# Kernel optimization log

Hardware: AMD Instinct MI355X
Metric: run time of the kernel (lower is better)

## Reference

```python
import jax, jax.numpy as jnp
import numpy as np

B, T, C, H = 2, 2048, 1024, 16
D = C // H
EPS = 1e-5
ROPE_BASE = 10000.0


def _rope_tables(t, d, base=ROPE_BASE):
    half = d // 2
    inv_freq = 1.0 / (base ** (jnp.arange(half, dtype=jnp.float32) / half))
    freqs = jnp.arange(t, dtype=jnp.float32)[:, None] * inv_freq[None, :]  # [T, D/2]
    emb = jnp.concatenate([freqs, freqs], axis=-1)  # [T, D]
    return jnp.cos(emb), jnp.sin(emb)


def _rotate_half(x):
    a, b = jnp.split(x, 2, axis=-1)
    return jnp.concatenate([-b, a], axis=-1)


def setup_inputs() -> dict:
    key = jax.random.key(0)
    k0, k1, k2 = jax.random.split(key, 3)
    s = 0.02  # typical init scale
    return {
        "x": jax.random.normal(k0, (B, T, C), jnp.float32),
        "attention_mask": jnp.ones((B, T), jnp.int32),
        "w_qkv": jax.random.normal(k1, (3 * C, C), jnp.float32) * s,
        "b_qkv": jnp.zeros((3 * C,), jnp.float32),
        "w_o": jax.random.normal(k2, (C, C), jnp.float32) * s,
        "b_o": jnp.zeros((C,), jnp.float32),
        "rms_w": jnp.ones((C,), jnp.float32),
    }


def reference(x, attention_mask, w_qkv, b_qkv, w_o, b_o, rms_w):
    b, t, c = x.shape
    h = H
    d = c // h
    # RMSNorm
    xn = x * jax.lax.rsqrt(jnp.mean(x * x, axis=-1, keepdims=True) + EPS) * rms_w
    # fused QKV projection -> [B, T, 3, H, D]
    qkv = (jnp.einsum('btc,oc->bto', xn, w_qkv) + b_qkv).reshape(b, t, 3, h, d)
    q, k, v = qkv[:, :, 0], qkv[:, :, 1], qkv[:, :, 2]
    # RoPE (position_ids = arange(T))
    cos, sin = _rope_tables(t, d)
    cos = cos[None, :, None, :]  # [1, T, 1, D]
    sin = sin[None, :, None, :]
    q = q * cos + _rotate_half(q) * sin
    k = k * cos + _rotate_half(k) * sin
    # causal attention (flash_attn_func semantics: scale 1/sqrt(d), causal)
    scores = jnp.einsum('bqhd,bkhd->bhqk', q, k) / jnp.sqrt(jnp.float32(d))
    causal = jnp.tril(jnp.ones((t, t), dtype=bool))
    scores = jnp.where(causal[None, None], scores, jnp.float32(-1e30))
    attn = jax.nn.softmax(scores, axis=-1)
    out = jnp.einsum('bhqk,bkhd->bqhd', attn, v).reshape(b, t, c)
    return jnp.einsum('btc,oc->bto', out, w_o) + b_o
```

## Files before the change

### kernel.cpp

```cpp
#include <hip/hip_runtime.h>
#include <math.h>

constexpr int Bb = 2;
constexpr int Tt = 2048;
constexpr int Cc = 1024;
constexpr int Hh = 16;
constexpr int M_ROWS = Bb * Tt;
constexpr float EPSV = 1e-5f;

typedef __attribute__((ext_vector_type(4))) float f32x4;
typedef __attribute__((ext_vector_type(8))) __bf16 bf16x8;
using u16 = unsigned short;

union Frag8 {
    u16 u[8];
    unsigned int ui[4];
    uint4 v;
    bf16x8 b;
};

__device__ __forceinline__ u16 f2bf(float f) {
    union { float f; unsigned int u; } c;
    c.f = f;
    unsigned int r = (c.u + 0x7fffu + ((c.u >> 16) & 1u)) >> 16;
    return (u16)r;
}
__device__ __forceinline__ float bf2f(u16 u) {
    union { unsigned int i; float f; } c;
    c.i = ((unsigned int)u) << 16;
    return c.f;
}

__device__ __forceinline__ void gload_lds16(const void* g, void* l) {
    __builtin_amdgcn_global_load_lds(
        (__attribute__((address_space(1))) void*)const_cast<void*>(g),
        (__attribute__((address_space(3))) void*)l, 16, 0, 0);
}

__global__ __launch_bounds__(64) void rope_tables_k(float* __restrict__ cosT,
                                                    float* __restrict__ sinT) {
    int tid = threadIdx.x;
    int t = blockIdx.x * 2 + (tid >> 5);
    int j = tid & 31;
    float inv = exp2f(-(float)j * (log2f(10000.0f) / 32.0f));
    float a = (float)t * inv;
    cosT[t * 32 + j] = cosf(a);
    sinT[t * 32 + j] = sinf(a);
}

__global__ __launch_bounds__(256) void f2bf_arr_k(const float* __restrict__ in,
                                                  u16* __restrict__ out) {
    int i = (blockIdx.x * 256 + threadIdx.x) * 4;
    float4 v = *(const float4*)&in[i];
    ushort4 o;
    o.x = f2bf(v.x); o.y = f2bf(v.y); o.z = f2bf(v.z); o.w = f2bf(v.w);
    *(ushort4*)&out[i] = o;
}

__global__ __launch_bounds__(256) void rmsnorm_k(const float* __restrict__ x,
                                                 const float* __restrict__ w,
                                                 u16* __restrict__ xn) {
    int row = blockIdx.x;
    int tid = threadIdx.x;
    const float* xr = x + (size_t)row * Cc;
    float4 v = *(const float4*)&xr[tid * 4];
    float ss = v.x * v.x + v.y * v.y + v.z * v.z + v.w * v.w;
    #pragma unroll
    for (int off = 32; off > 0; off >>= 1) ss += __shfl_down(ss, off);
    __shared__ float ws_[4];
    if ((tid & 63) == 0) ws_[tid >> 6] = ss;
    __syncthreads();
    float tot = ws_[0] + ws_[1] + ws_[2] + ws_[3];
    float r = rsqrtf(tot * (1.0f / (float)Cc) + EPSV);
    float4 wv = *(const float4*)&w[tid * 4];
    ushort4 o;
    o.x = f2bf(v.x * r * wv.x);
    o.y = f2bf(v.y * r * wv.y);
    o.z = f2bf(v.z * r * wv.z);
    o.w = f2bf(v.w * r * wv.w);
    *(ushort4*)&xn[(size_t)row * Cc + tid * 4] = o;
}

template<bool BF16OUT>
__global__ __launch_bounds__(256) void gemm_mfma_k(const u16* __restrict__ A,
                                                   const u16* __restrict__ W,
                                                   const float* __restrict__ bias,
                                                   void* __restrict__ Ov,
                                                   int M, int N, int K) {
    __shared__ __align__(16) u16 As[128 * 64];
    __shared__ __align__(16) u16 Bs[128 * 64];

    const int tid = threadIdx.x;
    const int w = tid >> 6;
    const int l = tid & 63;
    const int wr = w >> 1;
    const int wc = w & 1;
    const int q = l & 15;
    const int g = l >> 4;

    const int m0 = blockIdx.y * 128;
    const int n0 = blockIdx.x * 128;

    const int srow_in = l >> 3;
    const int p_chunk = l & 7;

    f32x4 acc[4][4];
    #pragma unroll
    for (int i = 0; i < 4; ++i)
        #pragma unroll
        for (int j = 0; j < 4; ++j)
            acc[i][j] = (f32x4){0.f, 0.f, 0.f, 0.f};

    const int nkt = K >> 6;
    for (int kt = 0; kt < nkt; ++kt) {
        const int k0 = kt << 6;
        __syncthreads();
        #pragma unroll
        for (int s = 0; s < 4; ++s) {
            int blk = s * 4 + w;
            int r = blk * 8 + srow_in;
            int c = p_chunk ^ (r & 7);
            gload_lds16(A + (size_t)(m0 + r) * K + k0 + c * 8, &As[blk * 512]);
            gload_lds16(W + (size_t)(n0 + r) * K + k0 + c * 8, &Bs[blk * 512]);
        }
        __syncthreads();

        #pragma unroll
        for (int kk = 0; kk < 2; ++kk) {
            Frag8 af[4], bf[4];
            const int ca = kk * 4 + g;
            #pragma unroll
            for (int i = 0; i < 4; ++i) {
                int ra = wr * 64 + i * 16 + q;
                af[i] = *(const Frag8*)&As[ra * 64 + ((ca ^ (ra & 7)) * 8)];
                int rb = wc * 64 + i * 16 + q;
                bf[i] = *(const Frag8*)&Bs[rb * 64 + ((ca ^ (rb & 7)) * 8)];
            }
            #pragma unroll
            for (int i = 0; i < 4; ++i)
                #pragma unroll
                for (int j = 0; j < 4; ++j)
                    acc[i][j] = __builtin_amdgcn_mfma_f32_16x16x32_bf16(
                        af[i].b, bf[j].b, acc[i][j], 0, 0, 0);
        }
    }

    #pragma unroll
    for (int i = 0; i < 4; ++i) {
        int row = m0 + wr * 64 + i * 16 + g * 4;
        #pragma unroll
        for (int j = 0; j < 4; ++j) {
            int col = n0 + wc * 64 + j * 16 + q;
            float bb = bias[col];
            #pragma unroll
            for (int r2 = 0; r2 < 4; ++r2) {
                float val = acc[i][j][r2] + bb;
                if (BF16OUT)
                    ((u16*)Ov)[(size_t)(row + r2) * N + col] = f2bf(val);
                else
                    ((float*)Ov)[(size_t)(row + r2) * N + col] = val;
            }
        }
    }
}

__global__ __launch_bounds__(256) void rope_pack_k(const u16* __restrict__ qkv,
                                                   const float* __restrict__ cosT,
                                                   const float* __restrict__ sinT,
                                                   u16* __restrict__ Qb,
                                                   u16* __restrict__ Kb,
                                                   u16* __restrict__ Vt) {
    const int t0 = blockIdx.x * 64;
    const int h = blockIdx.y, b = blockIdx.z;
    const int t = threadIdx.x;
    const int bh = b * Hh + h;
    __shared__ u16 Vs[64 * 64];
    constexpr float QSC = 0.125f * 1.44269504089f;

    {
        int row = t >> 2, d16 = (t & 3) * 16;
        const u16* vp = qkv + (size_t)(b * Tt + t0 + row) * 3072 + 2048 + h * 64 + d16;
        *(uint4*)&Vs[row * 64 + d16]     = *(const uint4*)vp;
        *(uint4*)&Vs[row * 64 + d16 + 8] = *(const uint4*)(vp + 8);
    }

    {
        int row = t >> 2, d0 = (t & 3) * 8;
        size_t rb = (size_t)(b * Tt + t0 + row) * 3072 + h * 64;
        const u16* qp = qkv + rb;
        const u16* kp = qkv + rb + 1024;
        Frag8 qlo, qhi, klo, khi;
        qlo.v = *(const uint4*)&qp[d0];
        qhi.v = *(const uint4*)&qp[d0 + 32];
        klo.v = *(const uint4*)&kp[d0];
        khi.v = *(const uint4*)&kp[d0 + 32];
        const float* cp = &cosT[(t0 + row) * 32 + d0];
        const float* sp = &sinT[(t0 + row) * 32 + d0];
        float4 c0 = *(const float4*)cp, c1 = *(const float4*)(cp + 4);
        float4 s0 = *(const float4*)sp, s1 = *(const float4*)(sp + 4);
        float cc[8] = {c0.x, c0.y, c0.z, c0.w, c1.x, c1.y, c1.z, c1.w};
        float ss[8] = {s0.x, s0.y, s0.z, s0.w, s1.x, s1.y, s1.z, s1.w};
        Frag8 oql, oqh, okl, okh;
        #pragma unroll
        for (int i = 0; i < 8; ++i) {
            float ql = bf2f(qlo.u[i]), qh = bf2f(qhi.u[i]);
            float kl = bf2f(klo.u[i]), kh = bf2f(khi.u[i]);
            oql.u[i] = f2bf((ql * cc[i] - qh * ss[i]) * QSC);
            oqh.u[i] = f2bf((qh * cc[i] + ql * ss[i]) * QSC);
            okl.u[i] = f2bf(kl * cc[i] - kh * ss[i]);
            okh.u[i] = f2bf(kh * cc[i] + kl * ss[i]);
        }
        u16* qd = Qb + ((size_t)bh * Tt + t0 + row) * 64;
        u16* kd = Kb + ((size_t)bh * Tt + t0 + row) * 64;
        *(uint4*)&qd[d0]      = oql.v;
        *(uint4*)&qd[d0 + 32] = oqh.v;
        *(uint4*)&kd[d0]      = okl.v;
        *(uint4*)&kd[d0 + 32] = okh.v;
    }
    __syncthreads();

    {
        int d = t >> 2, kq = (t & 3) * 16;
        Frag8 a, b2;
        #pragma unroll
        for (int j = 0; j < 16; ++j) {
            int slot = kq + j;
            int key = ((slot >> 5) * 2 + ((slot >> 2) & 1)) * 16
                    + ((slot >> 3) & 3) * 4 + (slot & 3);
            u16 vv = Vs[key * 64 + d];
            if (j < 8) a.u[j] = vv; else b2.u[j - 8] = vv;
        }
        u16* vd = Vt + ((size_t)bh * 64 + d) * Tt + t0 + kq;
        *(uint4*)&vd[0] = a.v;
        *(uint4*)&vd[8] = b2.v;
    }
}

__global__ __launch_bounds__(256) void attn_mfma_k(const u16* __restrict__ Qb,
                                                   const u16* __restrict__ Kb,
                                                   const u16* __restrict__ Vt,
                                                   u16* __restrict__ out) {
    const int i = blockIdx.x;
    int c, bh;
    if (i < 512) { c = 31 - (i >> 5); bh = i & 31; }
    else         { int k = i - 512; c = k >> 5; bh = k & 31; }
    const int b = bh >> 4, h = bh & 15;

    const int t = threadIdx.x;
    const int w = t >> 6;
    const int l = t & 63;
    const int q15 = l & 15;
    const int g2 = l >> 4;

    __shared__ __align__(16) u16 Ks[2][64 * 64];
    __shared__ __align__(16) u16 VTs[2][64 * 64];

    Frag8 qf[2];
    {
        int qrow = c * 64 + w * 16 + q15;
        const u16* qp = Qb + ((size_t)bh * Tt + qrow) * 64;
        qf[0] = *(const Frag8*)&qp[g2 * 8];
        qf[1] = *(const Frag8*)&qp[32 + g2 * 8];
    }

    Frag8 ones;
    #pragma unroll
    for (int e = 0; e < 8; ++e) ones.u[e] = 0x3F80;

    f32x4 acco[4];
    #pragma unroll
    for (int dg = 0; dg < 4; ++dg) acco[dg] = (f32x4){0.f, 0.f, 0.f, 0.f};
    f32x4 acc_l = (f32x4){0.f, 0.f, 0.f, 0.f};

    const int srow = l >> 3;
    const int cph = l & 7;
    const int cl = cph ^ srow;
    const u16* Kbase = Kb + (size_t)bh * Tt * 64;
    const u16* Vbase = Vt + (size_t)bh * 64 * Tt;

    #pragma unroll
    for (int iss = 0; iss < 2; ++iss) {
        int rr = w * 16 + iss * 8 + srow;
        gload_lds16(Kbase + (size_t)rr * 64 + cl * 8, &Ks[0][(w * 16 + iss * 8) * 64]);
        gload_lds16(Vbase + (size_t)rr * Tt + cl * 8, &VTs[0][(w * 16 + iss * 8) * 64]);
    }
    __syncthreads();

    int cur = 0;
    for (int j = 0; j <= c; ++j) {
        if (j < c) {
            #pragma unroll
            for (int iss = 0; iss < 2; ++iss) {
                int rr = w * 16 + iss * 8 + srow;
                gload_lds16(Kbase + (size_t)((j + 1) * 64 + rr) * 64 + cl * 8,
                            &Ks[cur ^ 1][(w * 16 + iss * 8) * 64]);
                gload_lds16(Vbase + (size_t)rr * Tt + (j + 1) * 64 + cl * 8,
                            &VTs[cur ^ 1][(w * 16 + iss * 8) * 64]);
            }
        }

        const u16* Kc = Ks[cur];
        const u16* Vc = VTs[cur];
        f32x4 sacc[4];
        __builtin_amdgcn_s_setprio(1);
        #pragma unroll
        for (int g = 0; g < 4; ++g) {
            sacc[g] = (f32x4){0.f, 0.f, 0.f, 0.f};
            int krow = g * 16 + q15;
            #pragma unroll
            for (int kk = 0; kk < 2; ++kk) {
                Frag8 kf = *(const Frag8*)&Kc[krow * 64 + (((kk * 4 + g2) ^ (krow & 7)) * 8)];
                sacc[g] = __builtin_amdgcn_mfma_f32_16x16x32_bf16(
                    kf.b, qf[kk].b, sacc[g], 0, 0, 0);
            }
        }
        __builtin_amdgcn_s_setprio(0);
        if (j == c) {
            #pragma unroll
            for (int g = 0; g < 4; ++g)
                #pragma unroll
                for (int r = 0; r < 4; ++r)
                    if (g * 16 + g2 * 4 + r > w * 16 + q15) sacc[g][r] = -1e30f;
        }

        Frag8 pa[2];
        #pragma unroll
        for (int kk = 0; kk < 2; ++kk)
            #pragma unroll
            for (int e = 0; e < 8; ++e)
                pa[kk].b[e] = (__bf16)exp2f(sacc[2 * kk + (e >> 2)][e & 3]);

        __builtin_amdgcn_s_setprio(1);
        acc_l = __builtin_amdgcn_mfma_f32_16x16x32_bf16(pa[0].b, ones.b, acc_l, 0, 0, 0);
        acc_l = __builtin_amdgcn_mfma_f32_16x16x32_bf16(pa[1].b, ones.b, acc_l, 0, 0, 0);
        #pragma unroll
        for (int dg = 0; dg < 4; ++dg) {
            int vrow = dg * 16 + q15;
            #pragma unroll
            for (int kk = 0; kk < 2; ++kk) {
                Frag8 vf = *(const Frag8*)&Vc[vrow * 64 + (((kk * 4 + g2) ^ (vrow & 7)) * 8)];
                acco[dg] = __builtin_amdgcn_mfma_f32_16x16x32_bf16(
                    pa[kk].b, vf.b, acco[dg], 0, 0, 0);
            }
        }
        __builtin_amdgcn_s_setprio(0);

        if (j < c) __syncthreads();
        cur ^= 1;
    }

    float lr[4];
    #pragma unroll
    for (int r = 0; r < 4; ++r) lr[r] = 1.f / acc_l[r];
    const int qbase = c * 64 + w * 16;
    #pragma unroll
    for (int dg = 0; dg < 4; ++dg)
        #pragma unroll
        for (int r = 0; r < 4; ++r)
            out[((size_t)(b * Tt + qbase + g2 * 4 + r)) * Cc + h * 64 + dg * 16 + q15] =
                f2bf(acco[dg][r] * lr[r]);
}

extern "C" void kernel_launch(void* const* d_in, const int* in_sizes, int n_in,
                              void* d_out, int out_size, void* d_ws, size_t ws_size,
                              hipStream_t stream) {
    const float* x      = (const float*)d_in[0];
    const float* w_qkv  = (const float*)d_in[2];
    const float* b_qkv  = (const float*)d_in[3];
    const float* w_o    = (const float*)d_in[4];
    const float* b_o    = (const float*)d_in[5];
    const float* rms_w  = (const float*)d_in[6];
    float* out = (float*)d_out;

    char* ws = (char*)d_ws;
    u16*   xn_bf   = (u16*)ws;
    u16*   Kb      = (u16*)(ws + (size_t)(8 << 20));
    u16*   Vt      = (u16*)(ws + (size_t)(16 << 20));
    u16*   Qb      = (u16*)(ws + (size_t)(24 << 20));
    u16*   qkvb    = (u16*)(ws + (size_t)(32 << 20));
    u16*   wqkv_bf = (u16*)(ws + (size_t)(56 << 20));
    u16*   wo_bf   = (u16*)(ws + (size_t)(62 << 20));
    float* cosT    = (float*)(ws + (size_t)(64 << 20));
    float* sinT    = (float*)(ws + (size_t)(64 << 20) + (1 << 18));
    u16*   attn_bf = xn_bf;

    rope_tables_k<<<dim3(Tt / 2), dim3(64), 0, stream>>>(cosT, sinT);
    f2bf_arr_k<<<dim3(3 * Cc * Cc / 1024), dim3(256), 0, stream>>>(w_qkv, wqkv_bf);
    f2bf_arr_k<<<dim3(Cc * Cc / 1024), dim3(256), 0, stream>>>(w_o, wo_bf);
    rmsnorm_k<<<dim3(M_ROWS), dim3(256), 0, stream>>>(x, rms_w, xn_bf);
    gemm_mfma_k<true><<<dim3(3 * Cc / 128, M_ROWS / 128), dim3(256), 0, stream>>>(
        xn_bf, wqkv_bf, b_qkv, qkvb, M_ROWS, 3 * Cc, Cc);
    rope_pack_k<<<dim3(Tt / 64, Hh, Bb), dim3(256), 0, stream>>>(
        qkvb, cosT, sinT, Qb, Kb, Vt);
    attn_mfma_k<<<dim3(1024), dim3(256), 0, stream>>>(Qb, Kb, Vt, attn_bf);
    gemm_mfma_k<false><<<dim3(Cc / 128, M_ROWS / 128), dim3(256), 0, stream>>>(
        attn_bf, wo_bf, b_o, out, M_ROWS, Cc, Cc);
}
```

Baseline: 135.6 us.

## Fuse RoPE and Q/K/V packing into QKV GEMM epilogue, swizzle block order

Removes the separate rope_pack kernel and the intermediate bf16 qkv buffer. The QKV GEMM epilogue now applies RoPE and the Q scale directly from accumulators and writes Q, K and the permuted transposed V layout that attention expects. The cos/sin tables are transposed to [j][t] so each lane can load four consecutive positions. Both GEMMs also use a 1D grid with an XCD-style block swizzle. The cost is scattered 2-byte stores in the epilogue instead of coalesced vector writes.

```diff
diff --git a/kernel.cpp b/kernel.cpp
--- a/kernel.cpp
+++ b/kernel.cpp
@@ -37,15 +37,15 @@
         (__attribute__((address_space(3))) void*)l, 16, 0, 0);
 }
 
-__global__ __launch_bounds__(64) void rope_tables_k(float* __restrict__ cosT,
-                                                    float* __restrict__ sinT) {
-    int tid = threadIdx.x;
-    int t = blockIdx.x * 2 + (tid >> 5);
-    int j = tid & 31;
+__global__ __launch_bounds__(256) void rope_tables_k(float* __restrict__ cos2,
+                                                     float* __restrict__ sin2) {
+    int lin = blockIdx.x * 256 + threadIdx.x;
+    int j = lin >> 11;
+    int t = lin & 2047;
     float inv = exp2f(-(float)j * (log2f(10000.0f) / 32.0f));
     float a = (float)t * inv;
-    cosT[t * 32 + j] = cosf(a);
-    sinT[t * 32 + j] = sinf(a);
+    cos2[lin] = cosf(a);
+    sin2[lin] = sinf(a);
 }
 
 __global__ __launch_bounds__(256) void f2bf_arr_k(const float* __restrict__ in,
@@ -81,14 +81,26 @@
     *(ushort4*)&xn[(size_t)row * Cc + tid * 4] = o;
 }
 
-template<bool BF16OUT>
+template<int MODE>
 __global__ __launch_bounds__(256) void gemm_mfma_k(const u16* __restrict__ A,
                                                    const u16* __restrict__ W,
                                                    const float* __restrict__ bias,
-                                                   void* __restrict__ Ov,
-                                                   int M, int N, int K) {
+                                                   float* __restrict__ Ov,
+                                                   int M, int N, int K,
+                                                   const float* __restrict__ cos2,
+                                                   const float* __restrict__ sin2,
+                                                   u16* __restrict__ Qb,
+                                                   u16* __restrict__ Kb,
+                                                   u16* __restrict__ Vt) {
     __shared__ __align__(16) u16 As[128 * 64];
     __shared__ __align__(16) u16 Bs[128 * 64];
+
+    const int nwg = gridDim.x;
+    const int lin = blockIdx.x;
+    const int swz = (lin & 7) * (nwg >> 3) + (lin >> 3);
+    const int mblk = M >> 7;
+    const int bx = swz / mblk, by = swz % mblk;
+    const int m0 = by * 128, n0 = bx * 128;
 
     const int tid = threadIdx.x;
     const int w = tid >> 6;
@@ -98,9 +110,6 @@
     const int q = l & 15;
     const int g = l >> 4;
 
-    const int m0 = blockIdx.y * 128;
-    const int n0 = blockIdx.x * 128;
-
     const int srow_in = l >> 3;
     const int p_chunk = l & 7;
 
@@ -145,94 +154,72 @@
         }
     }
 
-    #pragma unroll
-    for (int i = 0; i < 4; ++i) {
-        int row = m0 + wr * 64 + i * 16 + g * 4;
-        #pragma unroll
-        for (int j = 0; j < 4; ++j) {
-            int col = n0 + wc * 64 + j * 16 + q;
-            float bb = bias[col];
-            #pragma unroll
-            for (int r2 = 0; r2 < 4; ++r2) {
-                float val = acc[i][j][r2] + bb;
-                if (BF16OUT)
-                    ((u16*)Ov)[(size_t)(row + r2) * N + col] = f2bf(val);
-                else
-                    ((float*)Ov)[(size_t)(row + r2) * N + col] = val;
-            }
-        }
-    }
-}
-
-__global__ __launch_bounds__(256) void rope_pack_k(const u16* __restrict__ qkv,
-                                                   const float* __restrict__ cosT,
-                                                   const float* __restrict__ sinT,
-                                                   u16* __restrict__ Qb,
-                                                   u16* __restrict__ Kb,
-                                                   u16* __restrict__ Vt) {
-    const int t0 = blockIdx.x * 64;
-    const int h = blockIdx.y, b = blockIdx.z;
-    const int t = threadIdx.x;
-    const int bh = b * Hh + h;
-    __shared__ u16 Vs[64 * 64];
-    constexpr float QSC = 0.125f * 1.44269504089f;
-
-    {
-        int row = t >> 2, d16 = (t & 3) * 16;
-        const u16* vp = qkv + (size_t)(b * Tt + t0 + row) * 3072 + 2048 + h * 64 + d16;
-        *(uint4*)&Vs[row * 64 + d16]     = *(const uint4*)vp;
-        *(uint4*)&Vs[row * 64 + d16 + 8] = *(const uint4*)(vp + 8);
-    }
-
-    {
-        int row = t >> 2, d0 = (t & 3) * 8;
-        size_t rb = (size_t)(b * Tt + t0 + row) * 3072 + h * 64;
-        const u16* qp = qkv + rb;
-        const u16* kp = qkv + rb + 1024;
-        Frag8 qlo, qhi, klo, khi;
-        qlo.v = *(const uint4*)&qp[d0];
-        qhi.v = *(const uint4*)&qp[d0 + 32];
-        klo.v = *(const uint4*)&kp[d0];
-        khi.v = *(const uint4*)&kp[d0 + 32];
-        const float* cp = &cosT[(t0 + row) * 32 + d0];
-        const float* sp = &sinT[(t0 + row) * 32 + d0];
-        float4 c0 = *(const float4*)cp, c1 = *(const float4*)(cp + 4);
-        float4 s0 = *(const float4*)sp, s1 = *(const float4*)(sp + 4);
-        float cc[8] = {c0.x, c0.y, c0.z, c0.w, c1.x, c1.y, c1.z, c1.w};
-        float ss[8] = {s0.x, s0.y, s0.z, s0.w, s1.x, s1.y, s1.z, s1.w};
-        Frag8 oql, oqh, okl, okh;
-        #pragma unroll
-        for (int i = 0; i < 8; ++i) {
-            float ql = bf2f(qlo.u[i]), qh = bf2f(qhi.u[i]);
-            float kl = bf2f(klo.u[i]), kh = bf2f(khi.u[i]);
-            oql.u[i] = f2bf((ql * cc[i] - qh * ss[i]) * QSC);
-            oqh.u[i] = f2bf((qh * cc[i] + ql * ss[i]) * QSC);
-            okl.u[i] = f2bf(kl * cc[i] - kh * ss[i]);
-            okh.u[i] = f2bf(kh * cc[i] + kl * ss[i]);
-        }
-        u16* qd = Qb + ((size_t)bh * Tt + t0 + row) * 64;
-        u16* kd = Kb + ((size_t)bh * Tt + t0 + row) * 64;
-        *(uint4*)&qd[d0]      = oql.v;
-        *(uint4*)&qd[d0 + 32] = oqh.v;
-        *(uint4*)&kd[d0]      = okl.v;
-        *(uint4*)&kd[d0 + 32] = okh.v;
-    }
-    __syncthreads();
-
-    {
-        int d = t >> 2, kq = (t & 3) * 16;
-        Frag8 a, b2;
-        #pragma unroll
-        for (int j = 0; j < 16; ++j) {
-            int slot = kq + j;
-            int key = ((slot >> 5) * 2 + ((slot >> 2) & 1)) * 16
-                    + ((slot >> 3) & 3) * 4 + (slot & 3);
-            u16 vv = Vs[key * 64 + d];
-            if (j < 8) a.u[j] = vv; else b2.u[j - 8] = vv;
-        }
-        u16* vd = Vt + ((size_t)bh * 64 + d) * Tt + t0 + kq;
-        *(uint4*)&vd[0] = a.v;
-        *(uint4*)&vd[8] = b2.v;
+    float bj[4];
+    #pragma unroll
+    for (int j = 0; j < 4; ++j) bj[j] = bias[n0 + wc * 64 + j * 16 + q];
+
+    if (MODE == 0) {
+        #pragma unroll
+        for (int i = 0; i < 4; ++i) {
+            int row = m0 + wr * 64 + i * 16 + g * 4;
+            #pragma unroll
+            for (int j = 0; j < 4; ++j) {
+                int col = n0 + wc * 64 + j * 16 + q;
+                #pragma unroll
+                for (int r2 = 0; r2 < 4; ++r2)
+                    Ov[(size_t)(row + r2) * N + col] = acc[i][j][r2] + bj[j];
+            }
+        }
+    } else {
+        constexpr float QSC = 0.125f * 1.44269504089f;
+        const int ncb = n0 + wc * 64;
+        const int plane = ncb >> 10;
+        const int hh = (ncb & 1023) >> 6;
+        #pragma unroll
+        for (int i = 0; i < 4; ++i) {
+            int row0 = m0 + wr * 64 + i * 16 + g * 4;
+            int bb_ = row0 >> 11;
+            int t0 = row0 & 2047;
+            int bh2 = bb_ * Hh + hh;
+            if (plane == 2) {
+                int u0 = t0 & 63;
+                int slot0 = (u0 & 32) | ((u0 & 8) << 1) | ((u0 & 4) << 1) | ((u0 & 16) >> 2);
+                int tbase = (t0 & ~63) + slot0;
+                #pragma unroll
+                for (int j = 0; j < 4; ++j) {
+                    int d = j * 16 + q;
+                    ushort4 o;
+                    o.x = f2bf(acc[i][j][0] + bj[j]);
+                    o.y = f2bf(acc[i][j][1] + bj[j]);
+                    o.z = f2bf(acc[i][j][2] + bj[j]);
+                    o.w = f2bf(acc[i][j][3] + bj[j]);
+                    *(ushort4*)&Vt[((size_t)bh2 * 64 + d) * Tt + tbase] = o;
+                }
+            } else {
+                float4 c0 = *(const float4*)&cos2[q * Tt + t0];
+                float4 s0 = *(const float4*)&sin2[q * Tt + t0];
+                float4 c1 = *(const float4*)&cos2[(q + 16) * Tt + t0];
+                float4 s1 = *(const float4*)&sin2[(q + 16) * Tt + t0];
+                float cc0[4] = {c0.x, c0.y, c0.z, c0.w};
+                float ss0[4] = {s0.x, s0.y, s0.z, s0.w};
+                float cc1[4] = {c1.x, c1.y, c1.z, c1.w};
+                float ss1[4] = {s1.x, s1.y, s1.z, s1.w};
+                u16* dst = (plane == 0 ? Qb : Kb) + ((size_t)bh2 * Tt + t0) * 64;
+                const float scl = (plane == 0) ? QSC : 1.0f;
+                #pragma unroll
+                for (int r2 = 0; r2 < 4; ++r2) {
+                    float v0 = acc[i][0][r2] + bj[0];
+                    float v1 = acc[i][1][r2] + bj[1];
+                    float v2 = acc[i][2][r2] + bj[2];
+                    float v3 = acc[i][3][r2] + bj[3];
+                    u16* p = dst + (size_t)r2 * 64;
+                    p[q]      = f2bf((v0 * cc0[r2] - v2 * ss0[r2]) * scl);
+                    p[q + 16] = f2bf((v1 * cc1[r2] - v3 * ss1[r2]) * scl);
+                    p[q + 32] = f2bf((v2 * cc0[r2] + v0 * ss0[r2]) * scl);
+                    p[q + 48] = f2bf((v3 * cc1[r2] + v1 * ss1[r2]) * scl);
+                }
+            }
+        }
     }
 }
 
@@ -377,22 +364,21 @@
     u16*   Kb      = (u16*)(ws + (size_t)(8 << 20));
     u16*   Vt      = (u16*)(ws + (size_t)(16 << 20));
     u16*   Qb      = (u16*)(ws + (size_t)(24 << 20));
-    u16*   qkvb    = (u16*)(ws + (size_t)(32 << 20));
     u16*   wqkv_bf = (u16*)(ws + (size_t)(56 << 20));
     u16*   wo_bf   = (u16*)(ws + (size_t)(62 << 20));
-    float* cosT    = (float*)(ws + (size_t)(64 << 20));
-    float* sinT    = (float*)(ws + (size_t)(64 << 20) + (1 << 18));
+    float* cos2    = (float*)(ws + (size_t)(64 << 20));
+    float* sin2    = (float*)(ws + (size_t)(64 << 20) + (1 << 18));
     u16*   attn_bf = xn_bf;
 
-    rope_tables_k<<<dim3(Tt / 2), dim3(64), 0, stream>>>(cosT, sinT);
+    rope_tables_k<<<dim3(256), dim3(256), 0, stream>>>(cos2, sin2);
     f2bf_arr_k<<<dim3(3 * Cc * Cc / 1024), dim3(256), 0, stream>>>(w_qkv, wqkv_bf);
     f2bf_arr_k<<<dim3(Cc * Cc / 1024), dim3(256), 0, stream>>>(w_o, wo_bf);
     rmsnorm_k<<<dim3(M_ROWS), dim3(256), 0, stream>>>(x, rms_w, xn_bf);
-    gemm_mfma_k<true><<<dim3(3 * Cc / 128, M_ROWS / 128), dim3(256), 0, stream>>>(
-        xn_bf, wqkv_bf, b_qkv, qkvb, M_ROWS, 3 * Cc, Cc);
-    rope_pack_k<<<dim3(Tt / 64, Hh, Bb), dim3(256), 0, stream>>>(
-        qkvb, cosT, sinT, Qb, Kb, Vt);
+    gemm_mfma_k<1><<<dim3((3 * Cc / 128) * (M_ROWS / 128)), dim3(256), 0, stream>>>(
+        xn_bf, wqkv_bf, b_qkv, nullptr, M_ROWS, 3 * Cc, Cc,
+        cos2, sin2, Qb, Kb, Vt);
     attn_mfma_k<<<dim3(1024), dim3(256), 0, stream>>>(Qb, Kb, Vt, attn_bf);
-    gemm_mfma_k<false><<<dim3(Cc / 128, M_ROWS / 128), dim3(256), 0, stream>>>(
-        attn_bf, wo_bf, b_o, out, M_ROWS, Cc, Cc);
-}
+    gemm_mfma_k<0><<<dim3((Cc / 128) * (M_ROWS / 128)), dim3(256), 0, stream>>>(
+        attn_bf, wo_bf, b_o, out, M_ROWS, Cc, Cc,
+        nullptr, nullptr, nullptr, nullptr, nullptr);
+}
```

Result: no change. 136.0 us (+0.4%).

## Pair causal query tiles per attention block and merge prep kernels

Applied to the files above, without the earlier changes.

Each attention block now handles two query tiles, a long one (31-p) and its short mirror (p). Both share every K/V tile loaded into LDS, and the grid is halved to 512 balanced blocks. This cuts K/V global loads and evens out work across causal blocks, at the cost of roughly doubled accumulator registers and fewer blocks to fill the GPU. Separately, the rope-table and two weight-conversion kernels are fused into one launch to save launch overhead.

```diff
diff --git a/kernel.cpp b/kernel.cpp
--- a/kernel.cpp
+++ b/kernel.cpp
@@ -37,24 +37,33 @@
         (__attribute__((address_space(3))) void*)l, 16, 0, 0);
 }
 
-__global__ __launch_bounds__(64) void rope_tables_k(float* __restrict__ cosT,
-                                                    float* __restrict__ sinT) {
-    int tid = threadIdx.x;
-    int t = blockIdx.x * 2 + (tid >> 5);
-    int j = tid & 31;
-    float inv = exp2f(-(float)j * (log2f(10000.0f) / 32.0f));
-    float a = (float)t * inv;
-    cosT[t * 32 + j] = cosf(a);
-    sinT[t * 32 + j] = sinf(a);
-}
-
-__global__ __launch_bounds__(256) void f2bf_arr_k(const float* __restrict__ in,
-                                                  u16* __restrict__ out) {
-    int i = (blockIdx.x * 256 + threadIdx.x) * 4;
-    float4 v = *(const float4*)&in[i];
-    ushort4 o;
-    o.x = f2bf(v.x); o.y = f2bf(v.y); o.z = f2bf(v.z); o.w = f2bf(v.w);
-    *(ushort4*)&out[i] = o;
+__global__ __launch_bounds__(256) void prep_k(const float* __restrict__ w_qkv,
+                                              u16* __restrict__ wqkv_bf,
+                                              const float* __restrict__ w_o,
+                                              u16* __restrict__ wo_bf,
+                                              float* __restrict__ cosT,
+                                              float* __restrict__ sinT) {
+    int blk = blockIdx.x;
+    if (blk < 3072) {
+        int i = (blk * 256 + threadIdx.x) * 4;
+        float4 v = *(const float4*)&w_qkv[i];
+        ushort4 o;
+        o.x = f2bf(v.x); o.y = f2bf(v.y); o.z = f2bf(v.z); o.w = f2bf(v.w);
+        *(ushort4*)&wqkv_bf[i] = o;
+    } else if (blk < 4096) {
+        int i = ((blk - 3072) * 256 + threadIdx.x) * 4;
+        float4 v = *(const float4*)&w_o[i];
+        ushort4 o;
+        o.x = f2bf(v.x); o.y = f2bf(v.y); o.z = f2bf(v.z); o.w = f2bf(v.w);
+        *(ushort4*)&wo_bf[i] = o;
+    } else {
+        int lin = (blk - 4096) * 256 + threadIdx.x;
+        int tt = lin >> 5, j = lin & 31;
+        float inv = exp2f(-(float)j * (log2f(10000.0f) / 32.0f));
+        float a = (float)tt * inv;
+        cosT[lin] = cosf(a);
+        sinT[lin] = sinf(a);
+    }
 }
 
 __global__ __launch_bounds__(256) void rmsnorm_k(const float* __restrict__ x,
@@ -241,9 +250,9 @@
                                                    const u16* __restrict__ Vt,
                                                    u16* __restrict__ out) {
     const int i = blockIdx.x;
-    int c, bh;
-    if (i < 512) { c = 31 - (i >> 5); bh = i & 31; }
-    else         { int k = i - 512; c = k >> 5; bh = k & 31; }
+    const int p = i >> 5;
+    const int bh = i & 31;
+    const int cH = 31 - p, cL = p;
     const int b = bh >> 4, h = bh & 15;
 
     const int t = threadIdx.x;
@@ -255,110 +264,123 @@
     __shared__ __align__(16) u16 Ks[2][64 * 64];
     __shared__ __align__(16) u16 VTs[2][64 * 64];
 
-    Frag8 qf[2];
-    {
-        int qrow = c * 64 + w * 16 + q15;
+    Frag8 qf[2][2];
+    #pragma unroll
+    for (int s = 0; s < 2; ++s) {
+        int qrow = (s ? cL : cH) * 64 + w * 16 + q15;
         const u16* qp = Qb + ((size_t)bh * Tt + qrow) * 64;
-        qf[0] = *(const Frag8*)&qp[g2 * 8];
-        qf[1] = *(const Frag8*)&qp[32 + g2 * 8];
+        qf[s][0] = *(const Frag8*)&qp[g2 * 8];
+        qf[s][1] = *(const Frag8*)&qp[32 + g2 * 8];
     }
 
     Frag8 ones;
     #pragma unroll
     for (int e = 0; e < 8; ++e) ones.u[e] = 0x3F80;
 
-    f32x4 acco[4];
-    #pragma unroll
-    for (int dg = 0; dg < 4; ++dg) acco[dg] = (f32x4){0.f, 0.f, 0.f, 0.f};
-    f32x4 acc_l = (f32x4){0.f, 0.f, 0.f, 0.f};
+    f32x4 acco[2][4];
+    #pragma unroll
+    for (int s = 0; s < 2; ++s)
+        #pragma unroll
+        for (int dg = 0; dg < 4; ++dg) acco[s][dg] = (f32x4){0.f, 0.f, 0.f, 0.f};
+    f32x4 acc_l[2] = {(f32x4){0.f, 0.f, 0.f, 0.f}, (f32x4){0.f, 0.f, 0.f, 0.f}};
 
     const int srow = l >> 3;
     const int cph = l & 7;
-    const int cl = cph ^ srow;
+    const int xsw = cph ^ srow;
     const u16* Kbase = Kb + (size_t)bh * Tt * 64;
     const u16* Vbase = Vt + (size_t)bh * 64 * Tt;
 
     #pragma unroll
     for (int iss = 0; iss < 2; ++iss) {
         int rr = w * 16 + iss * 8 + srow;
-        gload_lds16(Kbase + (size_t)rr * 64 + cl * 8, &Ks[0][(w * 16 + iss * 8) * 64]);
-        gload_lds16(Vbase + (size_t)rr * Tt + cl * 8, &VTs[0][(w * 16 + iss * 8) * 64]);
+        gload_lds16(Kbase + (size_t)rr * 64 + xsw * 8, &Ks[0][(w * 16 + iss * 8) * 64]);
+        gload_lds16(Vbase + (size_t)rr * Tt + xsw * 8, &VTs[0][(w * 16 + iss * 8) * 64]);
     }
     __syncthreads();
 
     int cur = 0;
-    for (int j = 0; j <= c; ++j) {
-        if (j < c) {
+    for (int j = 0; j <= cH; ++j) {
+        if (j < cH) {
             #pragma unroll
             for (int iss = 0; iss < 2; ++iss) {
                 int rr = w * 16 + iss * 8 + srow;
-                gload_lds16(Kbase + (size_t)((j + 1) * 64 + rr) * 64 + cl * 8,
+                gload_lds16(Kbase + (size_t)((j + 1) * 64 + rr) * 64 + xsw * 8,
                             &Ks[cur ^ 1][(w * 16 + iss * 8) * 64]);
-                gload_lds16(Vbase + (size_t)rr * Tt + (j + 1) * 64 + cl * 8,
+                gload_lds16(Vbase + (size_t)rr * Tt + (j + 1) * 64 + xsw * 8,
                             &VTs[cur ^ 1][(w * 16 + iss * 8) * 64]);
             }
         }
 
         const u16* Kc = Ks[cur];
         const u16* Vc = VTs[cur];
-        f32x4 sacc[4];
-        __builtin_amdgcn_s_setprio(1);
-        #pragma unroll
-        for (int g = 0; g < 4; ++g) {
-            sacc[g] = (f32x4){0.f, 0.f, 0.f, 0.f};
-            int krow = g * 16 + q15;
-            #pragma unroll
-            for (int kk = 0; kk < 2; ++kk) {
-                Frag8 kf = *(const Frag8*)&Kc[krow * 64 + (((kk * 4 + g2) ^ (krow & 7)) * 8)];
-                sacc[g] = __builtin_amdgcn_mfma_f32_16x16x32_bf16(
-                    kf.b, qf[kk].b, sacc[g], 0, 0, 0);
-            }
-        }
-        __builtin_amdgcn_s_setprio(0);
-        if (j == c) {
-            #pragma unroll
-            for (int g = 0; g < 4; ++g)
+
+        #pragma unroll
+        for (int s = 0; s < 2; ++s) {
+            if (s == 1 && j > cL) continue;
+            const int cc = s ? cL : cH;
+
+            f32x4 sacc[4];
+            __builtin_amdgcn_s_setprio(1);
+            #pragma unroll
+            for (int g = 0; g < 4; ++g) {
+                sacc[g] = (f32x4){0.f, 0.f, 0.f, 0.f};
+                int krow = g * 16 + q15;
                 #pragma unroll
-                for (int r = 0; r < 4; ++r)
-                    if (g * 16 + g2 * 4 + r > w * 16 + q15) sacc[g][r] = -1e30f;
-        }
-
-        Frag8 pa[2];
-        #pragma unroll
-        for (int kk = 0; kk < 2; ++kk)
-            #pragma unroll
-            for (int e = 0; e < 8; ++e)
-                pa[kk].b[e] = (__bf16)exp2f(sacc[2 * kk + (e >> 2)][e & 3]);
-
-        __builtin_amdgcn_s_setprio(1);
-        acc_l = __builtin_amdgcn_mfma_f32_16x16x32_bf16(pa[0].b, ones.b, acc_l, 0, 0, 0);
-        acc_l = __builtin_amdgcn_mfma_f32_16x16x32_bf16(pa[1].b, ones.b, acc_l, 0, 0, 0);
-        #pragma unroll
-        for (int dg = 0; dg < 4; ++dg) {
-            int vrow = dg * 16 + q15;
-            #pragma unroll
-            for (int kk = 0; kk < 2; ++kk) {
-                Frag8 vf = *(const Frag8*)&Vc[vrow * 64 + (((kk * 4 + g2) ^ (vrow & 7)) * 8)];
-                acco[dg] = __builtin_amdgcn_mfma_f32_16x16x32_bf16(
-                    pa[kk].b, vf.b, acco[dg], 0, 0, 0);
-            }
-        }
-        __builtin_amdgcn_s_setprio(0);
-
-        if (j < c) __syncthreads();
+                for (int kk = 0; kk < 2; ++kk) {
+                    Frag8 kf = *(const Frag8*)&Kc[krow * 64 + (((kk * 4 + g2) ^ (krow & 7)) * 8)];
+                    sacc[g] = __builtin_amdgcn_mfma_f32_16x16x32_bf16(
+                        kf.b, qf[s][kk].b, sacc[g], 0, 0, 0);
+                }
+            }
+            __builtin_amdgcn_s_setprio(0);
+            if (j == cc) {
+                #pragma unroll
+                for (int g = 0; g < 4; ++g)
+                    #pragma unroll
+                    for (int r = 0; r < 4; ++r)
+                        if (g * 16 + g2 * 4 + r > w * 16 + q15) sacc[g][r] = -1e30f;
+            }
+
+            Frag8 pa[2];
+            #pragma unroll
+            for (int kk = 0; kk < 2; ++kk)
+                #pragma unroll
+                for (int e = 0; e < 8; ++e)
+                    pa[kk].b[e] = (__bf16)exp2f(sacc[2 * kk + (e >> 2)][e & 3]);
+
+            __builtin_amdgcn_s_setprio(1);
+            acc_l[s] = __builtin_amdgcn_mfma_f32_16x16x32_bf16(pa[0].b, ones.b, acc_l[s], 0, 0, 0);
+            acc_l[s] = __builtin_amdgcn_mfma_f32_16x16x32_bf16(pa[1].b, ones.b, acc_l[s], 0, 0, 0);
+            #pragma unroll
+            for (int dg = 0; dg < 4; ++dg) {
+                int vrow = dg * 16 + q15;
+                #pragma unroll
+                for (int kk = 0; kk < 2; ++kk) {
+                    Frag8 vf = *(const Frag8*)&Vc[vrow * 64 + (((kk * 4 + g2) ^ (vrow & 7)) * 8)];
+                    acco[s][dg] = __builtin_amdgcn_mfma_f32_16x16x32_bf16(
+                        pa[kk].b, vf.b, acco[s][dg], 0, 0, 0);
+                }
+            }
+            __builtin_amdgcn_s_setprio(0);
+        }
+
+        if (j < cH) __syncthreads();
         cur ^= 1;
     }
 
-    float lr[4];
-    #pragma unroll
-    for (int r = 0; r < 4; ++r) lr[r] = 1.f / acc_l[r];
-    const int qbase = c * 64 + w * 16;
-    #pragma unroll
-    for (int dg = 0; dg < 4; ++dg)
-        #pragma unroll
-        for (int r = 0; r < 4; ++r)
-            out[((size_t)(b * Tt + qbase + g2 * 4 + r)) * Cc + h * 64 + dg * 16 + q15] =
-                f2bf(acco[dg][r] * lr[r]);
+    #pragma unroll
+    for (int s = 0; s < 2; ++s) {
+        float lr[4];
+        #pragma unroll
+        for (int r = 0; r < 4; ++r) lr[r] = 1.f / acc_l[s][r];
+        const int qbase = (s ? cL : cH) * 64 + w * 16;
+        #pragma unroll
+        for (int dg = 0; dg < 4; ++dg)
+            #pragma unroll
+            for (int r = 0; r < 4; ++r)
+                out[((size_t)(b * Tt + qbase + g2 * 4 + r)) * Cc + h * 64 + dg * 16 + q15] =
+                    f2bf(acco[s][dg][r] * lr[r]);
+    }
 }
 
 extern "C" void kernel_launch(void* const* d_in, const int* in_sizes, int n_in,
@@ -384,15 +406,14 @@
     float* sinT    = (float*)(ws + (size_t)(64 << 20) + (1 << 18));
     u16*   attn_bf = xn_bf;
 
-    rope_tables_k<<<dim3(Tt / 2), dim3(64), 0, stream>>>(cosT, sinT);
-    f2bf_arr_k<<<dim3(3 * Cc * Cc / 1024), dim3(256), 0, stream>>>(w_qkv, wqkv_bf);
-    f2bf_arr_k<<<dim3(Cc * Cc / 1024), dim3(256), 0, stream>>>(w_o, wo_bf);
+    prep_k<<<dim3(4352), dim3(256), 0, stream>>>(w_qkv, wqkv_bf, w_o, wo_bf,
+                                                 cosT, sinT);
     rmsnorm_k<<<dim3(M_ROWS), dim3(256), 0, stream>>>(x, rms_w, xn_bf);
     gemm_mfma_k<true><<<dim3(3 * Cc / 128, M_ROWS / 128), dim3(256), 0, stream>>>(
         xn_bf, wqkv_bf, b_qkv, qkvb, M_ROWS, 3 * Cc, Cc);
     rope_pack_k<<<dim3(Tt / 64, Hh, Bb), dim3(256), 0, stream>>>(
         qkvb, cosT, sinT, Qb, Kb, Vt);
-    attn_mfma_k<<<dim3(1024), dim3(256), 0, stream>>>(Qb, Kb, Vt, attn_bf);
+    attn_mfma_k<<<dim3(512), dim3(256), 0, stream>>>(Qb, Kb, Vt, attn_bf);
     gemm_mfma_k<false><<<dim3(Cc / 128, M_ROWS / 128), dim3(256), 0, stream>>>(
         attn_bf, wo_bf, b_o, out, M_ROWS, Cc, Cc);
 }
```

Measured after the change: 131.3 us. -3.2%, faster.
